# Performance work log

Measured on AMD Instinct MI355X. Metric: run time of the kernel, lower is better.

## Reference

```python
import jax, jax.numpy as jnp
import numpy as np

D_MODEL, D_K, D_V, H = 1024, 64, 64, 16
LN_EPS = 1e-5


def setup_inputs() -> dict:
    key = jax.random.key(0)
    ks = jax.random.split(key, 16)
    B, NQ, NK = 2, 1024, 1024
    queries = jax.random.normal(ks[0], (B, NQ, D_MODEL), dtype=jnp.float32)
    keys = jax.random.normal(ks[1], (B, NK, D_MODEL), dtype=jnp.float32)
    values = jax.random.normal(ks[2], (B, NK, D_MODEL), dtype=jnp.float32)
    attention_mask = jax.random.randint(ks[3], (B, H, NQ, NK), 0, 2).astype(jnp.bool_)
    attention_weights = jax.random.uniform(ks[4], (B, H, NQ, NK), dtype=jnp.float32)
    # Linear params, stored (in, out) so x @ W + b
    def xavier(k, shape):
        lim = float(np.sqrt(6.0 / (shape[0] + shape[1])))
        return jax.random.uniform(k, shape, jnp.float32, -lim, lim)
    Wq = xavier(ks[5], (D_MODEL, H * D_K)); bq = jnp.zeros((H * D_K,), jnp.float32)
    Wk = xavier(ks[6], (D_MODEL, H * D_K)); bk = jnp.zeros((H * D_K,), jnp.float32)
    Wv = xavier(ks[7], (D_MODEL, H * D_V)); bv = jnp.zeros((H * D_V,), jnp.float32)
    Wo = xavier(ks[8], (H * D_V, D_MODEL)); bo = jnp.zeros((D_MODEL,), jnp.float32)
    gamma = jnp.ones((D_MODEL,), jnp.float32)
    beta = jnp.zeros((D_MODEL,), jnp.float32)
    return dict(queries=queries, keys=keys, values=values,
                attention_mask=attention_mask, attention_weights=attention_weights,
                Wq=Wq, bq=bq, Wk=Wk, bk=bk, Wv=Wv, bv=bv, Wo=Wo, bo=bo,
                gamma=gamma, beta=beta)


def layer_norm(x, gamma, beta):
    mu = jnp.mean(x, axis=-1, keepdims=True)
    var = jnp.mean(jnp.square(x - mu), axis=-1, keepdims=True)
    return (x - mu) * jax.lax.rsqrt(var + LN_EPS) * gamma + beta


def reference(queries, keys, values, attention_mask, attention_weights,
              Wq, bq, Wk, bk, Wv, bv, Wo, bo, gamma, beta):
    B, NQ, _ = queries.shape
    NK = keys.shape[1]
    q = (queries @ Wq + bq).reshape(B, NQ, H, D_K).transpose(0, 2, 1, 3)  # b h nq dk
    k = (keys @ Wk + bk).reshape(B, NK, H, D_K).transpose(0, 2, 1, 3)    # b h nk dk
    v = (values @ Wv + bv).reshape(B, NK, H, D_V).transpose(0, 2, 1, 3)  # b h nk dv
    att = jnp.einsum('bhqd,bhkd->bhqk', q, k) / jnp.sqrt(jnp.float32(D_K))
    att = att * attention_weights
    att = jnp.where(attention_mask, -jnp.inf, att)
    att = jax.nn.softmax(att, axis=-1)  # dropout is identity in eval
    out = jnp.einsum('bhqk,bhkd->bhqd', att, v)
    out = out.transpose(0, 2, 1, 3).reshape(B, NQ, H * D_V)
    out = out @ Wo + bo
    # post-LN residual (identity_map_reordering=False)
    return layer_norm(queries + out, gamma, beta)
```

## Files before the change

kernel.cpp:

```cpp
#include <hip/hip_runtime.h>
#include <hip/hip_bf16.h>
#include <math.h>

#define B_   2
#define H_   16
#define NSEQ 1024
#define DM   1024
#define DKV  64
#define NSPLIT 4
#define KPB  (NSEQ / NSPLIT)
#define LNEPS 1e-5f

typedef __attribute__((ext_vector_type(8))) short s16x8;
typedef __attribute__((ext_vector_type(4))) float f32x4;
typedef __attribute__((ext_vector_type(4))) unsigned u32x4;

__device__ inline short f2bf(float f) {
    __hip_bfloat16 h = __float2bfloat16(f);
    return *reinterpret_cast<short*>(&h);
}
__device__ inline float bf2f(short s) {
    unsigned u = ((unsigned)(unsigned short)s) << 16;
    return __uint_as_float(u);
}

__global__ void detect_mask(const unsigned* __restrict__ mask_words, int* __restrict__ flag) {
    unsigned f = 0;
    for (int i = 0; i < 256; ++i) f |= (mask_words[i] > 1u) ? 1u : 0u;
    *flag = (int)f;
}

__global__ __launch_bounds__(256) void cast3_bf16(
    const float* __restrict__ q, const float* __restrict__ k, const float* __restrict__ v,
    short* __restrict__ qo, short* __restrict__ ko, short* __restrict__ vo, int n) {
    const float* in = blockIdx.y == 0 ? q : (blockIdx.y == 1 ? k : v);
    short* out      = blockIdx.y == 0 ? qo : (blockIdx.y == 1 ? ko : vo);
    int i = (blockIdx.x * 256 + threadIdx.x) * 8;
    if (i >= n) return;
    f32x4 a = *(const f32x4*)(in + i);
    f32x4 b = *(const f32x4*)(in + i + 4);
    s16x8 o;
    o[0]=f2bf(a[0]); o[1]=f2bf(a[1]); o[2]=f2bf(a[2]); o[3]=f2bf(a[3]);
    o[4]=f2bf(b[0]); o[5]=f2bf(b[1]); o[6]=f2bf(b[2]); o[7]=f2bf(b[3]);
    *(s16x8*)(out + i) = o;
}

__global__ __launch_bounds__(256) void castT4_bf16(
    const float* __restrict__ w0, const float* __restrict__ w1,
    const float* __restrict__ w2, const float* __restrict__ w3,
    short* __restrict__ t0, short* __restrict__ t1,
    short* __restrict__ t2, short* __restrict__ t3) {
    const float* W = blockIdx.z == 0 ? w0 : (blockIdx.z == 1 ? w1 : (blockIdx.z == 2 ? w2 : w3));
    short* Wt      = blockIdx.z == 0 ? t0 : (blockIdx.z == 1 ? t1 : (blockIdx.z == 2 ? t2 : t3));
    __shared__ float tl[32][33];
    const int k0 = blockIdx.y * 32, n0 = blockIdx.x * 32;
    const int r = threadIdx.x >> 3, c4 = (threadIdx.x & 7) * 4;
    *(float4*)&tl[r][c4] = *(const float4*)(W + (size_t)(k0 + r) * DM + n0 + c4);
    __syncthreads();
    unsigned u0 = (unsigned short)f2bf(tl[c4+0][r]) | ((unsigned)(unsigned short)f2bf(tl[c4+1][r]) << 16);
    unsigned u1 = (unsigned short)f2bf(tl[c4+2][r]) | ((unsigned)(unsigned short)f2bf(tl[c4+3][r]) << 16);
    uint2 pk; pk.x = u0; pk.y = u1;
    *(uint2*)(Wt + (size_t)(n0 + r) * DM + k0 + c4) = pk;
}

__global__ __launch_bounds__(256) void gemm_bf16(
    const short* __restrict__ A, const short* __restrict__ Wt,
    const float* __restrict__ bias, const float* __restrict__ resid,
    void* __restrict__ outp, int mode)
{
    const int t  = threadIdx.x;
    const int wv = t >> 6, l = t & 63, lg = l >> 4, li = l & 15;
    const int wr = wv >> 1, wc = wv & 1;
    const int c0 = blockIdx.x * 64, m0 = blockIdx.y * 64;

    __shared__ short Asl[64 * 64];
    __shared__ short Bsl[64 * 64];

    f32x4 acc[2][2] = {};

    const int sr = t >> 2, scol = (t & 3) * 16;
    const int sw = (sr & 7) << 3;

    s16x8 a0 = *(const s16x8*)(A  + (size_t)(m0 + sr) * DM + scol);
    s16x8 a1 = *(const s16x8*)(A  + (size_t)(m0 + sr) * DM + scol + 8);
    s16x8 b0 = *(const s16x8*)(Wt + (size_t)(c0 + sr) * DM + scol);
    s16x8 b1 = *(const s16x8*)(Wt + (size_t)(c0 + sr) * DM + scol + 8);

    for (int k0 = 0; k0 < DM; k0 += 64) {
        __syncthreads();
        *(s16x8*)&Asl[sr * 64 + (scol ^ sw)]       = a0;
        *(s16x8*)&Asl[sr * 64 + ((scol + 8) ^ sw)] = a1;
        *(s16x8*)&Bsl[sr * 64 + (scol ^ sw)]       = b0;
        *(s16x8*)&Bsl[sr * 64 + ((scol + 8) ^ sw)] = b1;
        __syncthreads();
        if (k0 + 64 < DM) {
            a0 = *(const s16x8*)(A  + (size_t)(m0 + sr) * DM + k0 + 64 + scol);
            a1 = *(const s16x8*)(A  + (size_t)(m0 + sr) * DM + k0 + 64 + scol + 8);
            b0 = *(const s16x8*)(Wt + (size_t)(c0 + sr) * DM + k0 + 64 + scol);
            b1 = *(const s16x8*)(Wt + (size_t)(c0 + sr) * DM + k0 + 64 + scol + 8);
        }
        #pragma unroll
        for (int kh = 0; kh < 2; ++kh) {
            s16x8 af[2], bf[2];
            #pragma unroll
            for (int fi = 0; fi < 2; ++fi) {
                const int row = wr * 32 + fi * 16 + li;
                af[fi] = *(const s16x8*)&Asl[row * 64 + ((kh * 32 + lg * 8) ^ ((row & 7) << 3))];
            }
            #pragma unroll
            for (int fj = 0; fj < 2; ++fj) {
                const int row = wc * 32 + fj * 16 + li;
                bf[fj] = *(const s16x8*)&Bsl[row * 64 + ((kh * 32 + lg * 8) ^ ((row & 7) << 3))];
            }
            #pragma unroll
            for (int fi = 0; fi < 2; ++fi)
                #pragma unroll
                for (int fj = 0; fj < 2; ++fj)
                    acc[fi][fj] = __builtin_amdgcn_mfma_f32_16x16x32_bf16(af[fi], bf[fj], acc[fi][fj], 0, 0, 0);
        }
    }

    const int hh = c0 >> 6;
    #pragma unroll
    for (int fi = 0; fi < 2; ++fi) {
        #pragma unroll
        for (int j = 0; j < 4; ++j) {
            const int m = m0 + wr * 32 + fi * 16 + lg * 4 + j;
            const int bb = m >> 10, n = m & (NSEQ - 1);
            #pragma unroll
            for (int fj = 0; fj < 2; ++fj) {
                const int cc = wc * 32 + fj * 16 + li;
                const int c  = c0 + cc;
                float v = acc[fi][fj][j] + bias[c];
                if (mode == 1) {
                    ((short*)outp)[(((size_t)(bb * H_ + hh) * NSEQ) + n) * DKV + cc] = f2bf(v);
                } else if (mode == 2) {
                    ((short*)outp)[(((size_t)(bb * H_ + hh) * DKV) + cc) * NSEQ + n] = f2bf(v);
                } else {
                    float* of = (float*)outp;
                    of[(size_t)m * DM + c] = v + resid[(size_t)m * DM + c];
                }
            }
        }
    }
}

__global__ __launch_bounds__(256) void attn_split(
    const short* __restrict__ Qb, const short* __restrict__ Kb, const short* __restrict__ Vt,
    const void* __restrict__ mask, const float* __restrict__ wgt,
    const int* __restrict__ flagp, short* __restrict__ Opart,
    float* __restrict__ mpart, float* __restrict__ lpart)
{
    const int t  = threadIdx.x;
    const int wv = t >> 6;
    const int l  = t & 63;
    const int lg = l >> 4;
    const int li = l & 15;
    const int qt = blockIdx.x >> 2;
    const int sp = blockIdx.x & (NSPLIT-1);
    const int h  = blockIdx.y, b = blockIdx.z;
    const size_t bh = (size_t)b * H_ + h;
    const int qrow = qt*64 + wv*16 + li;
    const int kbase = sp * KPB;

    __shared__ short Plds[4][16][80];

    const short* Qp = Qb + (bh * NSEQ + qt*64 + wv*16) * DKV;
    const short* Kp = Kb + bh * NSEQ * DKV;
    const short* Vp = Vt + bh * DKV * NSEQ;
    const float* wrow = wgt + (bh * NSEQ + qrow) * NSEQ;
    const size_t moff = (bh * NSEQ + qrow) * NSEQ;
    const int mmode = *flagp;
    const unsigned* Mi = (const unsigned*)mask;
    const unsigned char* Mb = (const unsigned char*)mask;

    s16x8 qa[2];
    qa[0] = *(const s16x8*)(Qp + (size_t)li * DKV + lg*8);
    qa[1] = *(const s16x8*)(Qp + (size_t)li * DKV + 32 + lg*8);

    float m_run = -1e30f, l_run = 0.f;
    f32x4 oacc[4] = {};

    for (int kc = kbase; kc < kbase + KPB; kc += 64) {
        f32x4 sc[4] = {};
        #pragma unroll
        for (int dc = 0; dc < 2; ++dc)
            #pragma unroll
            for (int nt = 0; nt < 4; ++nt) {
                s16x8 kb = *(const s16x8*)(Kp + (size_t)(kc + nt*16 + li) * DKV + dc*32 + lg*8);
                sc[nt] = __builtin_amdgcn_mfma_f32_16x16x32_bf16(kb, qa[dc], sc[nt], 0, 0, 0);
            }

        s16x8 vf[8];
        #pragma unroll
        for (int kch = 0; kch < 2; ++kch)
            #pragma unroll
            for (int dt = 0; dt < 4; ++dt)
                vf[kch*4+dt] = *(const s16x8*)(Vp + (size_t)(dt*16 + li) * NSEQ + kc + kch*32 + lg*8);

        float sv[16];
        float cmax = -1e30f;
        #pragma unroll
        for (int nt = 0; nt < 4; ++nt) {
            const int k4 = kc + nt*16 + lg*4;
            f32x4 w4 = *(const f32x4*)(wrow + k4);
            unsigned mm[4];
            if (mmode) {
                unsigned u = *(const unsigned*)(Mb + moff + k4);
                mm[0] = u & 0xffu; mm[1] = (u >> 8) & 0xffu;
                mm[2] = (u >> 16) & 0xffu; mm[3] = u >> 24;
            } else {
                u32x4 mi = *(const u32x4*)(Mi + moff + k4);
                mm[0] = mi[0]; mm[1] = mi[1]; mm[2] = mi[2]; mm[3] = mi[3];
            }
            #pragma unroll
            for (int r = 0; r < 4; ++r) {
                float s = sc[nt][r] * 0.125f * w4[r];
                s = mm[r] ? -1e30f : s;
                sv[nt*4 + r] = s;
                cmax = fmaxf(cmax, s);
            }
        }
        cmax = fmaxf(cmax, __shfl_xor(cmax, 16));
        cmax = fmaxf(cmax, __shfl_xor(cmax, 32));
        const float mnew = fmaxf(m_run, cmax);
        const float factor = __expf(m_run - mnew);
        m_run = mnew;

        float csum = 0.f;
        #pragma unroll
        for (int nt = 0; nt < 4; ++nt) {
            float p0 = __expf(sv[nt*4+0] - mnew), p1 = __expf(sv[nt*4+1] - mnew);
            float p2 = __expf(sv[nt*4+2] - mnew), p3 = __expf(sv[nt*4+3] - mnew);
            csum += p0 + p1 + p2 + p3;
            unsigned u0 = (unsigned short)f2bf(p0) | ((unsigned)(unsigned short)f2bf(p1) << 16);
            unsigned u1 = (unsigned short)f2bf(p2) | ((unsigned)(unsigned short)f2bf(p3) << 16);
            uint2 pk; pk.x = u0; pk.y = u1;
            *(uint2*)&Plds[wv][li][nt*16 + lg*4] = pk;
        }
        csum += __shfl_xor(csum, 16);
        csum += __shfl_xor(csum, 32);
        l_run = l_run * factor + csum;

        float ffac[4];
        #pragma unroll
        for (int r = 0; r < 4; ++r) ffac[r] = __shfl(factor, lg*4 + r);
        #pragma unroll
        for (int dt = 0; dt < 4; ++dt)
            #pragma unroll
            for (int r = 0; r < 4; ++r)
                oacc[dt][r] *= ffac[r];

        #pragma unroll
        for (int kch = 0; kch < 2; ++kch) {
            s16x8 pa = *(const s16x8*)&Plds[wv][li][kch*32 + lg*8];
            #pragma unroll
            for (int dt = 0; dt < 4; ++dt)
                oacc[dt] = __builtin_amdgcn_mfma_f32_16x16x32_bf16(pa, vf[kch*4+dt], oacc[dt], 0, 0, 0);
        }
    }

    const size_t SBH = (size_t)B_ * H_ * NSEQ;
    if (lg == 0) {
        mpart[(size_t)sp * SBH + bh * NSEQ + qrow] = m_run;
        lpart[(size_t)sp * SBH + bh * NSEQ + qrow] = l_run;
    }
    #pragma unroll
    for (int dt = 0; dt < 4; ++dt)
        #pragma unroll
        for (int r = 0; r < 4; ++r)
            Opart[((size_t)sp * SBH + bh * NSEQ + qt*64 + wv*16 + lg*4 + r) * DKV + dt*16 + li]
                = f2bf(oacc[dt][r]);
}

__global__ __launch_bounds__(256) void attn_combine(
    const short* __restrict__ Opart, const float* __restrict__ mpart,
    const float* __restrict__ lpart, short* __restrict__ Ob)
{
    const size_t SBH = (size_t)B_ * H_ * NSEQ;
    const int R = blockIdx.x * 4 + (threadIdx.x >> 6);
    const int d = threadIdx.x & 63;
    const int bh = R >> 10, n = R & (NSEQ - 1);
    const int b = bh >> 4, h = bh & (H_ - 1);

    float ms[NSPLIT];
    float mstar = -1e30f;
    #pragma unroll
    for (int s = 0; s < NSPLIT; ++s) {
        ms[s] = mpart[(size_t)s * SBH + R];
        mstar = fmaxf(mstar, ms[s]);
    }
    float lstar = 0.f, acc = 0.f;
    #pragma unroll
    for (int s = 0; s < NSPLIT; ++s) {
        float w = __expf(ms[s] - mstar);
        lstar += w * lpart[(size_t)s * SBH + R];
        acc   += w * bf2f(Opart[((size_t)s * SBH + R) * DKV + d]);
    }
    Ob[((size_t)b * NSEQ + n) * DM + h * DKV + d] = f2bf(acc / lstar);
}

__global__ __launch_bounds__(256) void ln_kernel(
    const float* __restrict__ Y, const float* __restrict__ gamma,
    const float* __restrict__ beta, float* __restrict__ out)
{
    const int row = blockIdx.x;
    const int t = threadIdx.x;
    const float* y = Y + (size_t)row * DM;
    float4 x = *(const float4*)(y + t*4);
    __shared__ float red[4];
    float s = x.x + x.y + x.z + x.w;
    #pragma unroll
    for (int off = 32; off > 0; off >>= 1) s += __shfl_xor(s, off);
    if ((t & 63) == 0) red[t >> 6] = s;
    __syncthreads();
    float mean = (red[0]+red[1]+red[2]+red[3]) * (1.0f/DM);
    float d0 = x.x-mean, d1 = x.y-mean, d2 = x.z-mean, d3 = x.w-mean;
    float sq = d0*d0 + d1*d1 + d2*d2 + d3*d3;
    __syncthreads();
    #pragma unroll
    for (int off = 32; off > 0; off >>= 1) sq += __shfl_xor(sq, off);
    if ((t & 63) == 0) red[t >> 6] = sq;
    __syncthreads();
    float var = (red[0]+red[1]+red[2]+red[3]) * (1.0f/DM);
    float rstd = rsqrtf(var + LNEPS);
    int c = t * 4;
    float4 g  = *(const float4*)(gamma + c);
    float4 bb = *(const float4*)(beta + c);
    float4 o;
    o.x = d0*rstd*g.x + bb.x;
    o.y = d1*rstd*g.y + bb.y;
    o.z = d2*rstd*g.z + bb.z;
    o.w = d3*rstd*g.w + bb.w;
    *(float4*)(out + (size_t)row*DM + c) = o;
}

extern "C" void kernel_launch(void* const* d_in, const int* in_sizes, int n_in,
                              void* d_out, int out_size, void* d_ws, size_t ws_size,
                              hipStream_t stream)
{
    const float* queries = (const float*)d_in[0];
    const float* keys    = (const float*)d_in[1];
    const float* values  = (const float*)d_in[2];
    const void*  mask    = d_in[3];
    const float* wgt     = (const float*)d_in[4];
    const float* Wq = (const float*)d_in[5];  const float* bq = (const float*)d_in[6];
    const float* Wk = (const float*)d_in[7];  const float* bk = (const float*)d_in[8];
    const float* Wv = (const float*)d_in[9];  const float* bv = (const float*)d_in[10];
    const float* Wo = (const float*)d_in[11]; const float* bo = (const float*)d_in[12];
    const float* gamma = (const float*)d_in[13]; const float* beta = (const float*)d_in[14];
    float* out = (float*)d_out;

    const size_t SZ  = (size_t)B_ * NSEQ * DM;
    const size_t WSZ = (size_t)DM * DM;
    const size_t SBH = (size_t)B_ * H_ * NSEQ;

    char* ws = (char*)d_ws;
    int* flag  = (int*)ws;
    short* Qa  = (short*)(ws + 256);
    short* Ka  = Qa + SZ;
    short* Va  = Ka + SZ;
    short* Wtq = Va + SZ;
    short* Wtk = Wtq + WSZ;
    short* Wtv = Wtk + WSZ;
    short* Wto = Wtv + WSZ;
    short* Qh  = Wto + WSZ;
    short* Kh  = Qh + SZ;
    short* Vth = Kh + SZ;
    short* Opart = Vth + SZ;
    float* mpart = (float*)(Opart + (size_t)NSPLIT * SBH * DKV);
    float* lpart = mpart + (size_t)NSPLIT * SBH;
    short* Ob  = Va;
    float* Yb  = (float*)Qa;

    detect_mask<<<1, 1, 0, stream>>>((const unsigned*)mask, flag);
    cast3_bf16<<<dim3((int)(SZ/8/256), 3), 256, 0, stream>>>(queries, keys, values, Qa, Ka, Va, (int)SZ);
    castT4_bf16<<<dim3(32, 32, 4), 256, 0, stream>>>(Wq, Wk, Wv, Wo, Wtq, Wtk, Wtv, Wto);

    gemm_bf16<<<dim3(16, 32), 256, 0, stream>>>(Qa, Wtq, bq, nullptr, Qh, 1);
    gemm_bf16<<<dim3(16, 32), 256, 0, stream>>>(Ka, Wtk, bk, nullptr, Kh, 1);
    gemm_bf16<<<dim3(16, 32), 256, 0, stream>>>(Va, Wtv, bv, nullptr, Vth, 2);

    attn_split<<<dim3(16 * NSPLIT, H_, B_), 256, 0, stream>>>(Qh, Kh, Vth, mask, wgt, flag,
                                                              Opart, mpart, lpart);
    attn_combine<<<dim3((int)(SBH / 4)), 256, 0, stream>>>(Opart, mpart, lpart, Ob);

    gemm_bf16<<<dim3(16, 32), 256, 0, stream>>>(Ob, Wto, bo, queries, Yb, 0);
    ln_kernel<<<dim3(B_*NSEQ), 256, 0, stream>>>(Yb, gamma, beta, out);
}
```

Baseline: 193.6 us.

## Fuse input casts into GEMM loads and prepack mask-weights as bf16 tiles

Removes the separate fp32-to-bf16 cast kernel for queries/keys/values by converting inside the GEMM A-operand load. Adds a pre-pass that combines the attention mask and weights (pre-scaled by 1/sqrt(dk)) into a bf16 tensor laid out per 64-key chunk, with negative values marking masked entries, which attention then reads instead of the fp32 weights and mask. This halves the bytes attention reads for weights but adds a full extra read and write pass over the weight tensor, and quantizes the weights to bf16. The new path is taken only when the workspace is large enough.

```diff
diff --git a/kernel.cpp b/kernel.cpp
--- a/kernel.cpp
+++ b/kernel.cpp
@@ -9,9 +9,11 @@
 #define DKV  64
 #define NSPLIT 4
 #define KPB  (NSEQ / NSPLIT)
+#define WMCH 16
 #define LNEPS 1e-5f
 
 typedef __attribute__((ext_vector_type(8))) short s16x8;
+typedef __attribute__((ext_vector_type(4))) short s16x4;
 typedef __attribute__((ext_vector_type(4))) float f32x4;
 typedef __attribute__((ext_vector_type(4))) unsigned u32x4;
 
@@ -30,19 +32,42 @@
     *flag = (int)f;
 }
 
-__global__ __launch_bounds__(256) void cast3_bf16(
-    const float* __restrict__ q, const float* __restrict__ k, const float* __restrict__ v,
-    short* __restrict__ qo, short* __restrict__ ko, short* __restrict__ vo, int n) {
-    const float* in = blockIdx.y == 0 ? q : (blockIdx.y == 1 ? k : v);
-    short* out      = blockIdx.y == 0 ? qo : (blockIdx.y == 1 ? ko : vo);
-    int i = (blockIdx.x * 256 + threadIdx.x) * 8;
-    if (i >= n) return;
-    f32x4 a = *(const f32x4*)(in + i);
-    f32x4 b = *(const f32x4*)(in + i + 4);
-    s16x8 o;
-    o[0]=f2bf(a[0]); o[1]=f2bf(a[1]); o[2]=f2bf(a[2]); o[3]=f2bf(a[3]);
-    o[4]=f2bf(b[0]); o[5]=f2bf(b[1]); o[6]=f2bf(b[2]); o[7]=f2bf(b[3]);
-    *(s16x8*)(out + i) = o;
+__global__ __launch_bounds__(256) void wm_stream(
+    const void* __restrict__ mask, const float* __restrict__ wgt,
+    const int* __restrict__ flagp, short* __restrict__ wm)
+{
+    const int t = threadIdx.x, wv = t >> 6, l = t & 63;
+    const int qt = blockIdx.x, h = blockIdx.y, b = blockIdx.z;
+    const size_t bh = (size_t)b * H_ + h;
+    const int mmode = *flagp;
+    const unsigned char* Mb = (const unsigned char*)mask;
+    const unsigned* Mi = (const unsigned*)mask;
+
+    for (int rr = 0; rr < 16; ++rr) {
+        const int q = qt * 64 + wv * 16 + rr;
+        const size_t roff = (bh * NSEQ + q) * NSEQ;
+        #pragma unroll
+        for (int it = 0; it < 4; ++it) {
+            const int k = it * 256 + l * 4;
+            f32x4 w4 = *(const f32x4*)(wgt + roff + k);
+            unsigned m4[4];
+            if (mmode) {
+                uchar4 mb = *(const uchar4*)(Mb + roff + k);
+                m4[0] = mb.x; m4[1] = mb.y; m4[2] = mb.z; m4[3] = mb.w;
+            } else {
+                u32x4 mi = *(const u32x4*)(Mi + roff + k);
+                m4[0] = mi[0]; m4[1] = mi[1]; m4[2] = mi[2]; m4[3] = mi[3];
+            }
+            s16x4 o;
+            #pragma unroll
+            for (int r = 0; r < 4; ++r) {
+                float v = m4[r] ? -1.0f : w4[r] * 0.125f;
+                o[r] = f2bf(v);
+            }
+            const int ck = k >> 6, kk = k & 63;
+            *(s16x4*)(wm + (((size_t)bh * WMCH + ck) * NSEQ + q) * 64 + kk) = o;
+        }
+    }
 }
 
 __global__ __launch_bounds__(256) void castT4_bf16(
@@ -63,8 +88,26 @@
     *(uint2*)(Wt + (size_t)(n0 + r) * DM + k0 + c4) = pk;
 }
 
+template<int AF32>
+__device__ inline void loadA(const void* Av, size_t elemoff, s16x8& a0, s16x8& a1) {
+    if constexpr (AF32) {
+        const float* p = (const float*)Av + elemoff;
+        f32x4 v0 = *(const f32x4*)p,     v1 = *(const f32x4*)(p + 4);
+        f32x4 v2 = *(const f32x4*)(p + 8), v3 = *(const f32x4*)(p + 12);
+        a0[0]=f2bf(v0[0]); a0[1]=f2bf(v0[1]); a0[2]=f2bf(v0[2]); a0[3]=f2bf(v0[3]);
+        a0[4]=f2bf(v1[0]); a0[5]=f2bf(v1[1]); a0[6]=f2bf(v1[2]); a0[7]=f2bf(v1[3]);
+        a1[0]=f2bf(v2[0]); a1[1]=f2bf(v2[1]); a1[2]=f2bf(v2[2]); a1[3]=f2bf(v2[3]);
+        a1[4]=f2bf(v3[0]); a1[5]=f2bf(v3[1]); a1[6]=f2bf(v3[2]); a1[7]=f2bf(v3[3]);
+    } else {
+        const short* p = (const short*)Av + elemoff;
+        a0 = *(const s16x8*)p;
+        a1 = *(const s16x8*)(p + 8);
+    }
+}
+
+template<int AF32>
 __global__ __launch_bounds__(256) void gemm_bf16(
-    const short* __restrict__ A, const short* __restrict__ Wt,
+    const void* __restrict__ Av, const short* __restrict__ Wt,
     const float* __restrict__ bias, const float* __restrict__ resid,
     void* __restrict__ outp, int mode)
 {
@@ -81,8 +124,8 @@
     const int sr = t >> 2, scol = (t & 3) * 16;
     const int sw = (sr & 7) << 3;
 
-    s16x8 a0 = *(const s16x8*)(A  + (size_t)(m0 + sr) * DM + scol);
-    s16x8 a1 = *(const s16x8*)(A  + (size_t)(m0 + sr) * DM + scol + 8);
+    s16x8 a0, a1;
+    loadA<AF32>(Av, (size_t)(m0 + sr) * DM + scol, a0, a1);
     s16x8 b0 = *(const s16x8*)(Wt + (size_t)(c0 + sr) * DM + scol);
     s16x8 b1 = *(const s16x8*)(Wt + (size_t)(c0 + sr) * DM + scol + 8);
 
@@ -94,8 +137,7 @@
         *(s16x8*)&Bsl[sr * 64 + ((scol + 8) ^ sw)] = b1;
         __syncthreads();
         if (k0 + 64 < DM) {
-            a0 = *(const s16x8*)(A  + (size_t)(m0 + sr) * DM + k0 + 64 + scol);
-            a1 = *(const s16x8*)(A  + (size_t)(m0 + sr) * DM + k0 + 64 + scol + 8);
+            loadA<AF32>(Av, (size_t)(m0 + sr) * DM + k0 + 64 + scol, a0, a1);
             b0 = *(const s16x8*)(Wt + (size_t)(c0 + sr) * DM + k0 + 64 + scol);
             b1 = *(const s16x8*)(Wt + (size_t)(c0 + sr) * DM + k0 + 64 + scol + 8);
         }
@@ -145,8 +187,10 @@
     }
 }
 
+template<bool USE_WM>
 __global__ __launch_bounds__(256) void attn_split(
     const short* __restrict__ Qb, const short* __restrict__ Kb, const short* __restrict__ Vt,
+    const short* __restrict__ wm,
     const void* __restrict__ mask, const float* __restrict__ wgt,
     const int* __restrict__ flagp, short* __restrict__ Opart,
     float* __restrict__ mpart, float* __restrict__ lpart)
@@ -170,7 +214,8 @@
     const short* Vp = Vt + bh * DKV * NSEQ;
     const float* wrow = wgt + (bh * NSEQ + qrow) * NSEQ;
     const size_t moff = (bh * NSEQ + qrow) * NSEQ;
-    const int mmode = *flagp;
+    int mmode = 0;
+    if constexpr (!USE_WM) mmode = *flagp;
     const unsigned* Mi = (const unsigned*)mask;
     const unsigned char* Mb = (const unsigned char*)mask;
 
@@ -200,25 +245,41 @@
 
         float sv[16];
         float cmax = -1e30f;
-        #pragma unroll
-        for (int nt = 0; nt < 4; ++nt) {
-            const int k4 = kc + nt*16 + lg*4;
-            f32x4 w4 = *(const f32x4*)(wrow + k4);
-            unsigned mm[4];
-            if (mmode) {
-                unsigned u = *(const unsigned*)(Mb + moff + k4);
-                mm[0] = u & 0xffu; mm[1] = (u >> 8) & 0xffu;
-                mm[2] = (u >> 16) & 0xffu; mm[3] = u >> 24;
-            } else {
-                u32x4 mi = *(const u32x4*)(Mi + moff + k4);
-                mm[0] = mi[0]; mm[1] = mi[1]; mm[2] = mi[2]; mm[3] = mi[3];
-            }
-            #pragma unroll
-            for (int r = 0; r < 4; ++r) {
-                float s = sc[nt][r] * 0.125f * w4[r];
-                s = mm[r] ? -1e30f : s;
-                sv[nt*4 + r] = s;
-                cmax = fmaxf(cmax, s);
+        if constexpr (USE_WM) {
+            const short* wmp = wm + (((size_t)bh * WMCH + (kc >> 6)) * NSEQ + qrow) * 64;
+            #pragma unroll
+            for (int nt = 0; nt < 4; ++nt) {
+                s16x4 wmv = *(const s16x4*)(wmp + nt*16 + lg*4);
+                #pragma unroll
+                for (int r = 0; r < 4; ++r) {
+                    float wf = bf2f(wmv[r]);
+                    float s = sc[nt][r] * wf;
+                    s = (wf < 0.f) ? -1e30f : s;
+                    sv[nt*4 + r] = s;
+                    cmax = fmaxf(cmax, s);
+                }
+            }
+        } else {
+            #pragma unroll
+            for (int nt = 0; nt < 4; ++nt) {
+                const int k4 = kc + nt*16 + lg*4;
+                f32x4 w4 = *(const f32x4*)(wrow + k4);
+                unsigned mm[4];
+                if (mmode) {
+                    unsigned u = *(const unsigned*)(Mb + moff + k4);
+                    mm[0] = u & 0xffu; mm[1] = (u >> 8) & 0xffu;
+                    mm[2] = (u >> 16) & 0xffu; mm[3] = u >> 24;
+                } else {
+                    u32x4 mi = *(const u32x4*)(Mi + moff + k4);
+                    mm[0] = mi[0]; mm[1] = mi[1]; mm[2] = mi[2]; mm[3] = mi[3];
+                }
+                #pragma unroll
+                for (int r = 0; r < 4; ++r) {
+                    float s = sc[nt][r] * 0.125f * w4[r];
+                    s = mm[r] ? -1e30f : s;
+                    sv[nt*4 + r] = s;
+                    cmax = fmaxf(cmax, s);
+                }
             }
         }
         cmax = fmaxf(cmax, __shfl_xor(cmax, 16));
@@ -354,13 +415,11 @@
     const size_t SZ  = (size_t)B_ * NSEQ * DM;
     const size_t WSZ = (size_t)DM * DM;
     const size_t SBH = (size_t)B_ * H_ * NSEQ;
+    const size_t WMSZ = (size_t)B_ * H_ * WMCH * NSEQ * 64;
 
     char* ws = (char*)d_ws;
-    int* flag  = (int*)ws;
-    short* Qa  = (short*)(ws + 256);
-    short* Ka  = Qa + SZ;
-    short* Va  = Ka + SZ;
-    short* Wtq = Va + SZ;
+    int*   flag = (int*)ws;
+    short* Wtq = (short*)(ws + 256);
     short* Wtk = Wtq + WSZ;
     short* Wtv = Wtk + WSZ;
     short* Wto = Wtv + WSZ;
@@ -369,22 +428,30 @@
     short* Vth = Kh + SZ;
     short* Opart = Vth + SZ;
     float* mpart = (float*)(Opart + (size_t)NSPLIT * SBH * DKV);
-    float* lpart = mpart + (size_t)NSPLIT * SBH;
-    short* Ob  = Va;
-    float* Yb  = (float*)Qa;
+    float* lpart = mpart + NSPLIT * SBH;
+    short* Ob  = (short*)(lpart + NSPLIT * SBH);
+    float* Yb  = (float*)(Ob + SZ);
+    short* wm  = (short*)(Yb + SZ);
+    const size_t req = (size_t)((char*)(wm + WMSZ) - ws);
+    const bool use_wm = ws_size >= req;
 
     detect_mask<<<1, 1, 0, stream>>>((const unsigned*)mask, flag);
-    cast3_bf16<<<dim3((int)(SZ/8/256), 3), 256, 0, stream>>>(queries, keys, values, Qa, Ka, Va, (int)SZ);
     castT4_bf16<<<dim3(32, 32, 4), 256, 0, stream>>>(Wq, Wk, Wv, Wo, Wtq, Wtk, Wtv, Wto);
 
-    gemm_bf16<<<dim3(16, 32), 256, 0, stream>>>(Qa, Wtq, bq, nullptr, Qh, 1);
-    gemm_bf16<<<dim3(16, 32), 256, 0, stream>>>(Ka, Wtk, bk, nullptr, Kh, 1);
-    gemm_bf16<<<dim3(16, 32), 256, 0, stream>>>(Va, Wtv, bv, nullptr, Vth, 2);
-
-    attn_split<<<dim3(16 * NSPLIT, H_, B_), 256, 0, stream>>>(Qh, Kh, Vth, mask, wgt, flag,
-                                                              Opart, mpart, lpart);
+    gemm_bf16<1><<<dim3(16, 32), 256, 0, stream>>>(queries, Wtq, bq, nullptr, Qh, 1);
+    gemm_bf16<1><<<dim3(16, 32), 256, 0, stream>>>(keys,    Wtk, bk, nullptr, Kh, 1);
+    gemm_bf16<1><<<dim3(16, 32), 256, 0, stream>>>(values,  Wtv, bv, nullptr, Vth, 2);
+
+    if (use_wm) {
+        wm_stream<<<dim3(16, H_, B_), 256, 0, stream>>>(mask, wgt, flag, wm);
+        attn_split<true><<<dim3(16 * NSPLIT, H_, B_), 256, 0, stream>>>(
+            Qh, Kh, Vth, wm, mask, wgt, flag, Opart, mpart, lpart);
+    } else {
+        attn_split<false><<<dim3(16 * NSPLIT, H_, B_), 256, 0, stream>>>(
+            Qh, Kh, Vth, nullptr, mask, wgt, flag, Opart, mpart, lpart);
+    }
     attn_combine<<<dim3((int)(SBH / 4)), 256, 0, stream>>>(Opart, mpart, lpart, Ob);
 
-    gemm_bf16<<<dim3(16, 32), 256, 0, stream>>>(Ob, Wto, bo, queries, Yb, 0);
+    gemm_bf16<0><<<dim3(16, 32), 256, 0, stream>>>(Ob, Wto, bo, queries, Yb, 0);
     ln_kernel<<<dim3(B_*NSEQ), 256, 0, stream>>>(Yb, gamma, beta, out);
 }
```

New measurement: 261.8 us. 35.2% more time.

## Fuse input casts into one QKV GEMM and split attention into single-chunk blocks

Applied to the files above, without the earlier changes.

Removes the separate fp32-to-bf16 cast kernel by converting activations while loading them inside the projection GEMM. The Q, K and V projections now run as one launch over a concatenated weight buffer. Attention is split into 16 key chunks, so each block handles exactly one 64-key chunk with K and V preloaded, and the online-softmax rescaling is dropped in favour of the existing combine kernel. The trade-off is four times more partial output, max and sum data written and then read back by the combine step, plus a larger workspace.

```diff
diff --git a/kernel.cpp b/kernel.cpp
--- a/kernel.cpp
+++ b/kernel.cpp
@@ -7,8 +7,7 @@
 #define NSEQ 1024
 #define DM   1024
 #define DKV  64
-#define NSPLIT 4
-#define KPB  (NSEQ / NSPLIT)
+#define NSPLIT 16
 #define LNEPS 1e-5f
 
 typedef __attribute__((ext_vector_type(8))) short s16x8;
@@ -28,21 +27,6 @@
     unsigned f = 0;
     for (int i = 0; i < 256; ++i) f |= (mask_words[i] > 1u) ? 1u : 0u;
     *flag = (int)f;
-}
-
-__global__ __launch_bounds__(256) void cast3_bf16(
-    const float* __restrict__ q, const float* __restrict__ k, const float* __restrict__ v,
-    short* __restrict__ qo, short* __restrict__ ko, short* __restrict__ vo, int n) {
-    const float* in = blockIdx.y == 0 ? q : (blockIdx.y == 1 ? k : v);
-    short* out      = blockIdx.y == 0 ? qo : (blockIdx.y == 1 ? ko : vo);
-    int i = (blockIdx.x * 256 + threadIdx.x) * 8;
-    if (i >= n) return;
-    f32x4 a = *(const f32x4*)(in + i);
-    f32x4 b = *(const f32x4*)(in + i + 4);
-    s16x8 o;
-    o[0]=f2bf(a[0]); o[1]=f2bf(a[1]); o[2]=f2bf(a[2]); o[3]=f2bf(a[3]);
-    o[4]=f2bf(b[0]); o[5]=f2bf(b[1]); o[6]=f2bf(b[2]); o[7]=f2bf(b[3]);
-    *(s16x8*)(out + i) = o;
 }
 
 __global__ __launch_bounds__(256) void castT4_bf16(
@@ -63,26 +47,42 @@
     *(uint2*)(Wt + (size_t)(n0 + r) * DM + k0 + c4) = pk;
 }
 
-__global__ __launch_bounds__(256) void gemm_bf16(
-    const short* __restrict__ A, const short* __restrict__ Wt,
-    const float* __restrict__ bias, const float* __restrict__ resid,
-    void* __restrict__ outp, int mode)
+__device__ inline void loadAf32(const float* p, s16x8& a0, s16x8& a1) {
+    f32x4 v0 = *(const f32x4*)p,       v1 = *(const f32x4*)(p + 4);
+    f32x4 v2 = *(const f32x4*)(p + 8), v3 = *(const f32x4*)(p + 12);
+    a0[0]=f2bf(v0[0]); a0[1]=f2bf(v0[1]); a0[2]=f2bf(v0[2]); a0[3]=f2bf(v0[3]);
+    a0[4]=f2bf(v1[0]); a0[5]=f2bf(v1[1]); a0[6]=f2bf(v1[2]); a0[7]=f2bf(v1[3]);
+    a1[0]=f2bf(v2[0]); a1[1]=f2bf(v2[1]); a1[2]=f2bf(v2[2]); a1[3]=f2bf(v2[3]);
+    a1[4]=f2bf(v3[0]); a1[5]=f2bf(v3[1]); a1[6]=f2bf(v3[2]); a1[7]=f2bf(v3[3]);
+}
+
+__global__ __launch_bounds__(256) void gemm_qkv(
+    const float* __restrict__ qin, const float* __restrict__ kin, const float* __restrict__ vin,
+    const short* __restrict__ Wcat,
+    const float* __restrict__ bq, const float* __restrict__ bk, const float* __restrict__ bv,
+    short* __restrict__ Qh, short* __restrict__ Kh, short* __restrict__ Vth)
 {
     const int t  = threadIdx.x;
     const int wv = t >> 6, l = t & 63, lg = l >> 4, li = l & 15;
     const int wr = wv >> 1, wc = wv & 1;
-    const int c0 = blockIdx.x * 64, m0 = blockIdx.y * 64;
+    const int c0g = blockIdx.x * 64, m0 = blockIdx.y * 64;
+    const int sel = c0g >> 10;
+    const int c0  = c0g & 1023;
+    const float* A    = sel == 0 ? qin : (sel == 1 ? kin : vin);
+    const short* Wt   = Wcat + (size_t)sel * DM * DM;
+    const float* bias = sel == 0 ? bq : (sel == 1 ? bk : bv);
+    short* outp       = sel == 0 ? Qh : (sel == 1 ? Kh : Vth);
+    const int mode    = sel == 2 ? 2 : 1;
 
     __shared__ short Asl[64 * 64];
     __shared__ short Bsl[64 * 64];
 
     f32x4 acc[2][2] = {};
-
     const int sr = t >> 2, scol = (t & 3) * 16;
     const int sw = (sr & 7) << 3;
 
-    s16x8 a0 = *(const s16x8*)(A  + (size_t)(m0 + sr) * DM + scol);
-    s16x8 a1 = *(const s16x8*)(A  + (size_t)(m0 + sr) * DM + scol + 8);
+    s16x8 a0, a1;
+    loadAf32(A + (size_t)(m0 + sr) * DM + scol, a0, a1);
     s16x8 b0 = *(const s16x8*)(Wt + (size_t)(c0 + sr) * DM + scol);
     s16x8 b1 = *(const s16x8*)(Wt + (size_t)(c0 + sr) * DM + scol + 8);
 
@@ -94,8 +94,7 @@
         *(s16x8*)&Bsl[sr * 64 + ((scol + 8) ^ sw)] = b1;
         __syncthreads();
         if (k0 + 64 < DM) {
-            a0 = *(const s16x8*)(A  + (size_t)(m0 + sr) * DM + k0 + 64 + scol);
-            a1 = *(const s16x8*)(A  + (size_t)(m0 + sr) * DM + k0 + 64 + scol + 8);
+            loadAf32(A + (size_t)(m0 + sr) * DM + k0 + 64 + scol, a0, a1);
             b0 = *(const s16x8*)(Wt + (size_t)(c0 + sr) * DM + k0 + 64 + scol);
             b1 = *(const s16x8*)(Wt + (size_t)(c0 + sr) * DM + k0 + 64 + scol + 8);
         }
@@ -130,22 +129,110 @@
             #pragma unroll
             for (int fj = 0; fj < 2; ++fj) {
                 const int cc = wc * 32 + fj * 16 + li;
-                const int c  = c0 + cc;
-                float v = acc[fi][fj][j] + bias[c];
-                if (mode == 1) {
-                    ((short*)outp)[(((size_t)(bb * H_ + hh) * NSEQ) + n) * DKV + cc] = f2bf(v);
-                } else if (mode == 2) {
-                    ((short*)outp)[(((size_t)(bb * H_ + hh) * DKV) + cc) * NSEQ + n] = f2bf(v);
-                } else {
-                    float* of = (float*)outp;
-                    of[(size_t)m * DM + c] = v + resid[(size_t)m * DM + c];
-                }
-            }
-        }
-    }
-}
-
-__global__ __launch_bounds__(256) void attn_split(
+                float v = acc[fi][fj][j] + bias[c0 + cc];
+                if (mode == 1)
+                    outp[(((size_t)(bb * H_ + hh) * NSEQ) + n) * DKV + cc] = f2bf(v);
+                else
+                    outp[(((size_t)(bb * H_ + hh) * DKV) + cc) * NSEQ + n] = f2bf(v);
+            }
+        }
+    }
+}
+
+__global__ __launch_bounds__(256) void gemm_out(
+    const short* __restrict__ A, const short* __restrict__ Wt,
+    const float* __restrict__ bias, const float* __restrict__ resid,
+    float* __restrict__ outp)
+{
+    const int t  = threadIdx.x;
+    const int wv = t >> 6, l = t & 63, lg = l >> 4, li = l & 15;
+    const int wr = wv >> 1, wc = wv & 1;
+    const int c0 = blockIdx.x * 64, m0 = blockIdx.y * 64;
+
+    __shared__ short Asl[64 * 64];
+    __shared__ short Bsl[64 * 64];
+
+    f32x4 acc[2][2] = {};
+    const int sr = t >> 2, scol = (t & 3) * 16;
+    const int sw = (sr & 7) << 3;
+
+    s16x8 a0 = *(const s16x8*)(A + (size_t)(m0 + sr) * DM + scol);
+    s16x8 a1 = *(const s16x8*)(A + (size_t)(m0 + sr) * DM + scol + 8);
+    s16x8 b0 = *(const s16x8*)(Wt + (size_t)(c0 + sr) * DM + scol);
+    s16x8 b1 = *(const s16x8*)(Wt + (size_t)(c0 + sr) * DM + scol + 8);
+
+    for (int k0 = 0; k0 < DM; k0 += 64) {
+        __syncthreads();
+        *(s16x8*)&Asl[sr * 64 + (scol ^ sw)]       = a0;
+        *(s16x8*)&Asl[sr * 64 + ((scol + 8) ^ sw)] = a1;
+        *(s16x8*)&Bsl[sr * 64 + (scol ^ sw)]       = b0;
+        *(s16x8*)&Bsl[sr * 64 + ((scol + 8) ^ sw)] = b1;
+        __syncthreads();
+        if (k0 + 64 < DM) {
+            a0 = *(const s16x8*)(A + (size_t)(m0 + sr) * DM + k0 + 64 + scol);
+            a1 = *(const s16x8*)(A + (size_t)(m0 + sr) * DM + k0 + 64 + scol + 8);
+            b0 = *(const s16x8*)(Wt + (size_t)(c0 + sr) * DM + k0 + 64 + scol);
+            b1 = *(const s16x8*)(Wt + (size_t)(c0 + sr) * DM + k0 + 64 + scol + 8);
+        }
+        #pragma unroll
+        for (int kh = 0; kh < 2; ++kh) {
+            s16x8 af[2], bf[2];
+            #pragma unroll
+            for (int fi = 0; fi < 2; ++fi) {
+                const int row = wr * 32 + fi * 16 + li;
+                af[fi] = *(const s16x8*)&Asl[row * 64 + ((kh * 32 + lg * 8) ^ ((row & 7) << 3))];
+            }
+            #pragma unroll
+            for (int fj = 0; fj < 2; ++fj) {
+                const int row = wc * 32 + fj * 16 + li;
+                bf[fj] = *(const s16x8*)&Bsl[row * 64 + ((kh * 32 + lg * 8) ^ ((row & 7) << 3))];
+            }
+            #pragma unroll
+            for (int fi = 0; fi < 2; ++fi)
+                #pragma unroll
+                for (int fj = 0; fj < 2; ++fj)
+                    acc[fi][fj] = __builtin_amdgcn_mfma_f32_16x16x32_bf16(af[fi], bf[fj], acc[fi][fj], 0, 0, 0);
+        }
+    }
+
+    #pragma unroll
+    for (int fi = 0; fi < 2; ++fi) {
+        #pragma unroll
+        for (int j = 0; j < 4; ++j) {
+            const int m = m0 + wr * 32 + fi * 16 + lg * 4 + j;
+            #pragma unroll
+            for (int fj = 0; fj < 2; ++fj) {
+                const int c = c0 + wc * 32 + fj * 16 + li;
+                outp[(size_t)m * DM + c] = acc[fi][fj][j] + bias[c] + resid[(size_t)m * DM + c];
+            }
+        }
+    }
+}
+
+__device__ __forceinline__ void wload(
+    const float* __restrict__ wrow, const unsigned char* __restrict__ Mb,
+    const unsigned* __restrict__ Mi, size_t moff, int mmode, int kc, int lg, f32x4* wq)
+{
+    #pragma unroll
+    for (int nt = 0; nt < 4; ++nt) {
+        const int k4 = kc + nt*16 + lg*4;
+        f32x4 w4 = *(const f32x4*)(wrow + k4);
+        unsigned mm[4];
+        if (mmode) {
+            unsigned u = *(const unsigned*)(Mb + moff + k4);
+            mm[0]=u&0xffu; mm[1]=(u>>8)&0xffu; mm[2]=(u>>16)&0xffu; mm[3]=u>>24;
+        } else {
+            u32x4 mi = *(const u32x4*)(Mi + moff + k4);
+            mm[0]=mi[0]; mm[1]=mi[1]; mm[2]=mi[2]; mm[3]=mi[3];
+        }
+        f32x4 o;
+        #pragma unroll
+        for (int r = 0; r < 4; ++r) o[r] = mm[r] ? -1.0f : 0.125f * w4[r];
+        wq[nt] = o;
+    }
+}
+
+__global__ __launch_bounds__(256) void attn_one(
     const short* __restrict__ Qb, const short* __restrict__ Kb, const short* __restrict__ Vt,
     const void* __restrict__ mask, const float* __restrict__ wgt,
     const int* __restrict__ flagp, short* __restrict__ Opart,
@@ -156,12 +243,12 @@
     const int l  = t & 63;
     const int lg = l >> 4;
     const int li = l & 15;
-    const int qt = blockIdx.x >> 2;
+    const int qt = blockIdx.x >> 4;
     const int sp = blockIdx.x & (NSPLIT-1);
     const int h  = blockIdx.y, b = blockIdx.z;
     const size_t bh = (size_t)b * H_ + h;
     const int qrow = qt*64 + wv*16 + li;
-    const int kbase = sp * KPB;
+    const int kc = sp * 64;
 
     __shared__ short Plds[4][16][80];
 
@@ -178,92 +265,72 @@
     qa[0] = *(const s16x8*)(Qp + (size_t)li * DKV + lg*8);
     qa[1] = *(const s16x8*)(Qp + (size_t)li * DKV + 32 + lg*8);
 
-    float m_run = -1e30f, l_run = 0.f;
+    s16x8 kf[8];
+    #pragma unroll
+    for (int dc = 0; dc < 2; ++dc)
+        #pragma unroll
+        for (int nt = 0; nt < 4; ++nt)
+            kf[dc*4+nt] = *(const s16x8*)(Kp + (size_t)(kc + nt*16 + li) * DKV + dc*32 + lg*8);
+
+    s16x8 vf[8];
+    #pragma unroll
+    for (int kch = 0; kch < 2; ++kch)
+        #pragma unroll
+        for (int dt = 0; dt < 4; ++dt)
+            vf[kch*4+dt] = *(const s16x8*)(Vp + (size_t)(dt*16 + li) * NSEQ + kc + kch*32 + lg*8);
+
+    f32x4 wq[4];
+    wload(wrow, Mb, Mi, moff, mmode, kc, lg, wq);
+
+    f32x4 sc[4] = {};
+    #pragma unroll
+    for (int dc = 0; dc < 2; ++dc)
+        #pragma unroll
+        for (int nt = 0; nt < 4; ++nt)
+            sc[nt] = __builtin_amdgcn_mfma_f32_16x16x32_bf16(kf[dc*4+nt], qa[dc], sc[nt], 0, 0, 0);
+
+    float sv[16];
+    float cmax = -1e30f;
+    #pragma unroll
+    for (int nt = 0; nt < 4; ++nt)
+        #pragma unroll
+        for (int r = 0; r < 4; ++r) {
+            float wf = wq[nt][r];
+            float s = sc[nt][r] * wf;
+            s = (wf < 0.f) ? -1e30f : s;
+            sv[nt*4 + r] = s;
+            cmax = fmaxf(cmax, s);
+        }
+    cmax = fmaxf(cmax, __shfl_xor(cmax, 16));
+    cmax = fmaxf(cmax, __shfl_xor(cmax, 32));
+
+    float csum = 0.f;
+    #pragma unroll
+    for (int nt = 0; nt < 4; ++nt) {
+        float p0 = __expf(sv[nt*4+0] - cmax), p1 = __expf(sv[nt*4+1] - cmax);
+        float p2 = __expf(sv[nt*4+2] - cmax), p3 = __expf(sv[nt*4+3] - cmax);
+        csum += p0 + p1 + p2 + p3;
+        unsigned u0 = (unsigned short)f2bf(p0) | ((unsigned)(unsigned short)f2bf(p1) << 16);
+        unsigned u1 = (unsigned short)f2bf(p2) | ((unsigned)(unsigned short)f2bf(p3) << 16);
+        uint2 pk; pk.x = u0; pk.y = u1;
+        *(uint2*)&Plds[wv][li][nt*16 + lg*4] = pk;
+    }
+    csum += __shfl_xor(csum, 16);
+    csum += __shfl_xor(csum, 32);
+
     f32x4 oacc[4] = {};
-
-    for (int kc = kbase; kc < kbase + KPB; kc += 64) {
-        f32x4 sc[4] = {};
-        #pragma unroll
-        for (int dc = 0; dc < 2; ++dc)
-            #pragma unroll
-            for (int nt = 0; nt < 4; ++nt) {
-                s16x8 kb = *(const s16x8*)(Kp + (size_t)(kc + nt*16 + li) * DKV + dc*32 + lg*8);
-                sc[nt] = __builtin_amdgcn_mfma_f32_16x16x32_bf16(kb, qa[dc], sc[nt], 0, 0, 0);
-            }
-
-        s16x8 vf[8];
-        #pragma unroll
-        for (int kch = 0; kch < 2; ++kch)
-            #pragma unroll
-            for (int dt = 0; dt < 4; ++dt)
-                vf[kch*4+dt] = *(const s16x8*)(Vp + (size_t)(dt*16 + li) * NSEQ + kc + kch*32 + lg*8);
-
-        float sv[16];
-        float cmax = -1e30f;
-        #pragma unroll
-        for (int nt = 0; nt < 4; ++nt) {
-            const int k4 = kc + nt*16 + lg*4;
-            f32x4 w4 = *(const f32x4*)(wrow + k4);
-            unsigned mm[4];
-            if (mmode) {
-                unsigned u = *(const unsigned*)(Mb + moff + k4);
-                mm[0] = u & 0xffu; mm[1] = (u >> 8) & 0xffu;
-                mm[2] = (u >> 16) & 0xffu; mm[3] = u >> 24;
-            } else {
-                u32x4 mi = *(const u32x4*)(Mi + moff + k4);
-                mm[0] = mi[0]; mm[1] = mi[1]; mm[2] = mi[2]; mm[3] = mi[3];
-            }
-            #pragma unroll
-            for (int r = 0; r < 4; ++r) {
-                float s = sc[nt][r] * 0.125f * w4[r];
-                s = mm[r] ? -1e30f : s;
-                sv[nt*4 + r] = s;
-                cmax = fmaxf(cmax, s);
-            }
-        }
-        cmax = fmaxf(cmax, __shfl_xor(cmax, 16));
-        cmax = fmaxf(cmax, __shfl_xor(cmax, 32));
-        const float mnew = fmaxf(m_run, cmax);
-        const float factor = __expf(m_run - mnew);
-        m_run = mnew;
-
-        float csum = 0.f;
-        #pragma unroll
-        for (int nt = 0; nt < 4; ++nt) {
-            float p0 = __expf(sv[nt*4+0] - mnew), p1 = __expf(sv[nt*4+1] - mnew);
-            float p2 = __expf(sv[nt*4+2] - mnew), p3 = __expf(sv[nt*4+3] - mnew);
-            csum += p0 + p1 + p2 + p3;
-            unsigned u0 = (unsigned short)f2bf(p0) | ((unsigned)(unsigned short)f2bf(p1) << 16);
-            unsigned u1 = (unsigned short)f2bf(p2) | ((unsigned)(unsigned short)f2bf(p3) << 16);
-            uint2 pk; pk.x = u0; pk.y = u1;
-            *(uint2*)&Plds[wv][li][nt*16 + lg*4] = pk;
-        }
-        csum += __shfl_xor(csum, 16);
-        csum += __shfl_xor(csum, 32);
-        l_run = l_run * factor + csum;
-
-        float ffac[4];
-        #pragma unroll
-        for (int r = 0; r < 4; ++r) ffac[r] = __shfl(factor, lg*4 + r);
+    #pragma unroll
+    for (int kch = 0; kch < 2; ++kch) {
+        s16x8 pa = *(const s16x8*)&Plds[wv][li][kch*32 + lg*8];
         #pragma unroll
         for (int dt = 0; dt < 4; ++dt)
-            #pragma unroll
-            for (int r = 0; r < 4; ++r)
-                oacc[dt][r] *= ffac[r];
-
-        #pragma unroll
-        for (int kch = 0; kch < 2; ++kch) {
-            s16x8 pa = *(const s16x8*)&Plds[wv][li][kch*32 + lg*8];
-            #pragma unroll
-            for (int dt = 0; dt < 4; ++dt)
-                oacc[dt] = __builtin_amdgcn_mfma_f32_16x16x32_bf16(pa, vf[kch*4+dt], oacc[dt], 0, 0, 0);
-        }
+            oacc[dt] = __builtin_amdgcn_mfma_f32_16x16x32_bf16(pa, vf[kch*4+dt], oacc[dt], 0, 0, 0);
     }
 
     const size_t SBH = (size_t)B_ * H_ * NSEQ;
     if (lg == 0) {
-        mpart[(size_t)sp * SBH + bh * NSEQ + qrow] = m_run;
-        lpart[(size_t)sp * SBH + bh * NSEQ + qrow] = l_run;
+        mpart[(size_t)sp * SBH + bh * NSEQ + qrow] = cmax;
+        lpart[(size_t)sp * SBH + bh * NSEQ + qrow] = csum;
     }
     #pragma unroll
     for (int dt = 0; dt < 4; ++dt)
@@ -356,11 +423,8 @@
     const size_t SBH = (size_t)B_ * H_ * NSEQ;
 
     char* ws = (char*)d_ws;
-    int* flag  = (int*)ws;
-    short* Qa  = (short*)(ws + 256);
-    short* Ka  = Qa + SZ;
-    short* Va  = Ka + SZ;
-    short* Wtq = Va + SZ;
+    int*   flag = (int*)ws;
+    short* Wtq = (short*)(ws + 256);
     short* Wtk = Wtq + WSZ;
     short* Wtv = Wtk + WSZ;
     short* Wto = Wtv + WSZ;
@@ -369,22 +433,20 @@
     short* Vth = Kh + SZ;
     short* Opart = Vth + SZ;
     float* mpart = (float*)(Opart + (size_t)NSPLIT * SBH * DKV);
-    float* lpart = mpart + (size_t)NSPLIT * SBH;
-    short* Ob  = Va;
-    float* Yb  = (float*)Qa;
+    float* lpart = mpart + NSPLIT * SBH;
+    short* Ob  = (short*)(lpart + NSPLIT * SBH);
+    float* Yb  = (float*)Opart;
 
     detect_mask<<<1, 1, 0, stream>>>((const unsigned*)mask, flag);
-    cast3_bf16<<<dim3((int)(SZ/8/256), 3), 256, 0, stream>>>(queries, keys, values, Qa, Ka, Va, (int)SZ);
     castT4_bf16<<<dim3(32, 32, 4), 256, 0, stream>>>(Wq, Wk, Wv, Wo, Wtq, Wtk, Wtv, Wto);
 
-    gemm_bf16<<<dim3(16, 32), 256, 0, stream>>>(Qa, Wtq, bq, nullptr, Qh, 1);
-    gemm_bf16<<<dim3(16, 32), 256, 0, stream>>>(Ka, Wtk, bk, nullptr, Kh, 1);
-    gemm_bf16<<<dim3(16, 32), 256, 0, stream>>>(Va, Wtv, bv, nullptr, Vth, 2);
-
-    attn_split<<<dim3(16 * NSPLIT, H_, B_), 256, 0, stream>>>(Qh, Kh, Vth, mask, wgt, flag,
-                                                              Opart, mpart, lpart);
+    gemm_qkv<<<dim3(48, 32), 256, 0, stream>>>(queries, keys, values, Wtq,
+                                               bq, bk, bv, Qh, Kh, Vth);
+
+    attn_one<<<dim3(16 * NSPLIT, H_, B_), 256, 0, stream>>>(
+        Qh, Kh, Vth, mask, wgt, flag, Opart, mpart, lpart);
     attn_combine<<<dim3((int)(SBH / 4)), 256, 0, stream>>>(Opart, mpart, lpart, Ob);
 
-    gemm_bf16<<<dim3(16, 32), 256, 0, stream>>>(Ob, Wto, bo, queries, Yb, 0);
+    gemm_out<<<dim3(16, 32), 256, 0, stream>>>(Ob, Wto, bo, queries, Yb);
     ln_kernel<<<dim3(B_*NSEQ), 256, 0, stream>>>(Yb, gamma, beta, out);
 }
```

Measured after the change: 227.7 us. +17.6%, slower.
